# Kernel tuning notes

Measured on AMD Instinct MI355X. Metric: run time of the kernel, lower is better.

Reference implementation:

```python
import jax, jax.numpy as jnp
import numpy as np

NEG = -1e30  # effective -inf in float32, safe under logaddexp grads
EPS = 1e-7   # keras.backend.epsilon()


def _ctc_loss(y_pred, y_true):
    """Faithful port of keras.backend.ctc_batch_cost with full-length
    input_length=T and label_length=L (as the CTCLayer sets them).
    y_pred: [B, T, C] post-softmax probabilities; blank = C-1.
    y_true: [B, L] int labels in [0, C-1).
    Returns loss [B, 1].
    """
    logp = jnp.log(y_pred + EPS)            # keras takes log(prob + eps)
    B, T, C = y_pred.shape
    L = y_true.shape[1]
    S = 2 * L + 1
    blank = C - 1

    # Extended label sequence: blank, l1, blank, l2, ..., blank  -> [B, S]
    ext = jnp.full((B, S), blank, dtype=y_true.dtype).at[:, 1::2].set(y_true)
    # Per-time emission log-probs of extended symbols: [B, T, S]
    lp_ext = jnp.take_along_axis(logp, ext[:, None, :], axis=2)

    # Skip transition s-2 -> s allowed when ext[s] != blank and ext[s] != ext[s-2]
    prev2_ext = jnp.pad(ext[:, :-2], ((0, 0), (2, 0)), constant_values=-1)
    allow_skip = (ext != blank) & (ext != prev2_ext)  # [B, S]

    # alpha init at t=0
    alpha = jnp.full((B, S), NEG, dtype=logp.dtype)
    alpha = alpha.at[:, 0].set(lp_ext[:, 0, 0]).at[:, 1].set(lp_ext[:, 0, 1])

    def step(alpha, lp_t):
        shift1 = jnp.pad(alpha[:, :-1], ((0, 0), (1, 0)), constant_values=NEG)
        shift2 = jnp.pad(alpha[:, :-2], ((0, 0), (2, 0)), constant_values=NEG)
        shift2 = jnp.where(allow_skip, shift2, NEG)
        new = jnp.logaddexp(jnp.logaddexp(alpha, shift1), shift2) + lp_t
        return new, None

    lp_seq = jnp.moveaxis(lp_ext[:, 1:, :], 1, 0)  # [T-1, B, S]
    alpha, _ = jax.lax.scan(step, alpha, lp_seq)

    # Terminate in final blank or final label
    loss = -jnp.logaddexp(alpha[:, S - 1], alpha[:, S - 2])  # [B]
    return loss[:, None]  # keras returns [B, 1]


def setup_inputs() -> dict:
    key = jax.random.key(0)
    k1, k2 = jax.random.split(key)
    B, T, C, L = 256, 256, 1000, 64
    y_true = jax.random.randint(k1, (B, L), 0, C - 1, dtype=jnp.int64)
    logits = jax.random.normal(k2, (B, T, C), dtype=jnp.float32)
    y_pred = jax.nn.softmax(logits, axis=-1)  # module expects softmax probs
    return {"y_true": y_true, "y_pred": y_pred}


def reference(y_true, y_pred):
    return _ctc_loss(y_pred, y_true)
```

## Files before the change

### kernel.cpp

```cpp
#include <hip/hip_runtime.h>


#define T_    256
#define C_    1000
#define L_    64
#define BLANK 999
#define NEGF  (-1e30f)
#define EPSF  (1e-7f)
#define RS    68
#define CK    64
#define NV    17

__global__ __launch_bounds__(256)
void ctc_gather_kernel(const int* __restrict__ y_true,
                       const float* __restrict__ y_pred,
                       float* __restrict__ lp) {
    const int wave = threadIdx.x >> 6;
    const int lane = threadIdx.x & 63;
    const int pair = blockIdx.x * 4 + wave;
    const int b = pair >> 8;

    const int lab = y_true[b * L_ + lane];
    const float* __restrict__ row = y_pred + (size_t)pair * C_;
    float* __restrict__ orow = lp + (size_t)pair * RS;

    float v = row[lab];
    orow[1 + lane] = __logf(v + EPSF);
    if (lane == 0) {
        orow[0] = __logf(row[BLANK] + EPSF);
    }
}

__global__ __launch_bounds__(64)
void ctc_scan_kernel(const int* __restrict__ y_true,
                     const float* __restrict__ lp,
                     float* __restrict__ out) {
    __shared__ float sbuf[2][CK * RS];

    const int b    = blockIdx.x;
    const int lane = threadIdx.x;

    const float* __restrict__ lrow = lp + (size_t)b * T_ * RS;

    const int lab   = y_true[b * L_ + lane];
    const int labm1 = __shfl_up(lab, 1, 64);
    const bool allow = (lane > 0) && (lab != labm1);

    float aE = NEGF, aO = NEGF, aL = NEGF;

    float4 va[NV], vb[NV];

    auto loadChunk = [&](int c, float4 (&v)[NV]) {
        const float4* g = (const float4*)(lrow + (size_t)c * CK * RS);
        #pragma unroll
        for (int k = 0; k < NV; ++k) v[k] = g[k * 64 + lane];
    };
    auto writeChunk = [&](int sel, float4 (&v)[NV]) {
        float4* d = (float4*)&sbuf[sel][0];
        #pragma unroll
        for (int k = 0; k < NV; ++k) d[k * 64 + lane] = v[k];
    };

    auto step = [&](float lpB, float lpL) {
        float upO = __shfl_up(aO, 1, 64);
        if (lane == 0) upO = NEGF;
        float mE = fmaxf(aE, upO);
        float nE = mE + __logf(__expf(aE - mE) + __expf(upO - mE)) + lpB;
        float sk = allow ? upO : NEGF;
        float mO = fmaxf(fmaxf(aO, aE), sk);
        float nO = mO + __logf(__expf(aO - mO) + __expf(aE - mO) +
                               __expf(sk - mO)) + lpL;
        float mL = fmaxf(aL, aO);
        float nL2 = mL + __logf(__expf(aL - mL) + __expf(aO - mL)) + lpB;
        aE = nE; aO = nO; aL = nL2;
    };

    auto scanChunk = [&](int sel, int rlo) {
        const float* B = &sbuf[sel][0];
        float rB0 = B[rlo * RS],       rL0 = B[rlo * RS + 1 + lane];
        float rB1 = B[(rlo + 1) * RS], rL1 = B[(rlo + 1) * RS + 1 + lane];
        for (int j = rlo; j < CK; ++j) {
            float lpB = rB0, lpL = rL0;
            rB0 = rB1; rL0 = rL1;
            int nr = j + 2; if (nr > CK - 1) nr = CK - 1;
            rB1 = B[nr * RS]; rL1 = B[nr * RS + 1 + lane];
            step(lpB, lpL);
        }
    };

    loadChunk(0, va); writeChunk(0, va);
    loadChunk(1, vb);

    aE = (lane == 0) ? sbuf[0][0] : NEGF;
    aO = (lane == 0) ? sbuf[0][1] : NEGF;

    scanChunk(0, 1);
    writeChunk(1, vb);
    loadChunk(2, va);
    scanChunk(1, 0);
    writeChunk(0, va);
    loadChunk(3, vb);
    scanChunk(0, 0);
    writeChunk(1, vb);
    scanChunk(1, 0);

    if (lane == 63) {
        float m = fmaxf(aL, aO);
        out[b] = -(m + __logf(__expf(aL - m) + __expf(aO - m)));
    }
}

extern "C" void kernel_launch(void* const* d_in, const int* in_sizes, int n_in,
                              void* d_out, int out_size, void* d_ws, size_t ws_size,
                              hipStream_t stream) {
    const int*   y_true = (const int*)d_in[0];
    const float* y_pred = (const float*)d_in[1];
    float*       out    = (float*)d_out;
    float*       lp     = (float*)d_ws;
    (void)in_sizes; (void)n_in; (void)ws_size; (void)out_size;

    ctc_gather_kernel<<<dim3((256 * 256) / 4), dim3(256), 0, stream>>>(y_true, y_pred, lp);
    ctc_scan_kernel<<<dim3(256), dim3(64), 0, stream>>>(y_true, lp, out);
}
```

Before: 401.2 us.

## Replace scattered label gather with coalesced row streaming and class-to-slot map

The gather kernel, which read one scattered element per label from each probability row, is replaced by an extract kernel that streams whole rows with coalesced float4 loads. It writes log-probs only for classes present in the label set, using a per-batch byte map from class to a deduplicated slot. The scan kernel then reads each label's log-prob through its first-occurrence slot index, with blank at slot 64. This trades many uncoalesced 4-byte reads for full-row bandwidth (about 1000 floats per row), plus a serial duplicate search in both kernels.

Result: slower. 434.6 us (+8.3%).

```diff
diff --git a/kernel.cpp b/kernel.cpp
--- a/kernel.cpp
+++ b/kernel.cpp
@@ -10,24 +10,55 @@
 #define RS    68
 #define CK    64
 #define NV    17
+#define RPB   32
 
 __global__ __launch_bounds__(256)
-void ctc_gather_kernel(const int* __restrict__ y_true,
-                       const float* __restrict__ y_pred,
-                       float* __restrict__ lp) {
-    const int wave = threadIdx.x >> 6;
-    const int lane = threadIdx.x & 63;
-    const int pair = blockIdx.x * 4 + wave;
-    const int b = pair >> 8;
+void ctc_extract_kernel(const int* __restrict__ y_true,
+                        const float* __restrict__ y_pred,
+                        float* __restrict__ V) {
+    __shared__ int          slab[64];
+    __shared__ unsigned int sm32[256];
 
-    const int lab = y_true[b * L_ + lane];
-    const float* __restrict__ row = y_pred + (size_t)pair * C_;
-    float* __restrict__ orow = lp + (size_t)pair * RS;
+    const int tid = threadIdx.x;
+    const int b   = blockIdx.x >> 3;
+    const int t0  = (blockIdx.x & 7) * RPB;
 
-    float v = row[lab];
-    orow[1 + lane] = __logf(v + EPSF);
-    if (lane == 0) {
-        orow[0] = __logf(row[BLANK] + EPSF);
+    sm32[tid] = 0xFFFFFFFFu;
+    if (tid < 64) slab[tid] = y_true[b * L_ + tid];
+    __syncthreads();
+    if (tid < 64) {
+        const int myl = slab[tid];
+        int fp = tid;
+        for (int j = 0; j < 64; ++j) { if (slab[j] == myl) { fp = j; break; } }
+        if (fp == tid) ((unsigned char*)sm32)[myl] = (unsigned char)tid;
+    }
+    if (tid == 0) ((unsigned char*)sm32)[BLANK] = 64;
+    __syncthreads();
+
+    const bool act = tid < 250;
+    const unsigned int sm = sm32[tid];
+    const float* __restrict__ base = y_pred + ((size_t)b * T_ + t0) * C_;
+
+    for (int r0 = 0; r0 < RPB; r0 += 4) {
+        float4 v[4];
+        #pragma unroll
+        for (int q = 0; q < 4; ++q) {
+            const float* row = base + (size_t)(r0 + q) * C_;
+            v[q] = act ? ((const float4*)row)[tid]
+                       : make_float4(0.f, 0.f, 0.f, 0.f);
+        }
+        if (act && sm != 0xFFFFFFFFu) {
+            #pragma unroll
+            for (int q = 0; q < 4; ++q) {
+                float* orow = V + (size_t)(b * T_ + t0 + r0 + q) * RS;
+                const float vals[4] = { v[q].x, v[q].y, v[q].z, v[q].w };
+                #pragma unroll
+                for (int e = 0; e < 4; ++e) {
+                    const unsigned int sl = (sm >> (8 * e)) & 0xFFu;
+                    if (sl != 0xFFu) orow[sl] = __logf(vals[e] + EPSF);
+                }
+            }
+        }
     }
 }
 
@@ -45,6 +76,12 @@
     const int lab   = y_true[b * L_ + lane];
     const int labm1 = __shfl_up(lab, 1, 64);
     const bool allow = (lane > 0) && (lab != labm1);
+
+    int fp = 64;
+    for (int j = 0; j < 64; ++j) {
+        const int lj = __shfl(lab, j, 64);
+        if (fp == 64 && lj == lab) fp = j;
+    }
 
     float aE = NEGF, aO = NEGF, aL = NEGF;
 
@@ -77,13 +114,13 @@
 
     auto scanChunk = [&](int sel, int rlo) {
         const float* B = &sbuf[sel][0];
-        float rB0 = B[rlo * RS],       rL0 = B[rlo * RS + 1 + lane];
-        float rB1 = B[(rlo + 1) * RS], rL1 = B[(rlo + 1) * RS + 1 + lane];
+        float rB0 = B[rlo * RS + 64],       rL0 = B[rlo * RS + fp];
+        float rB1 = B[(rlo + 1) * RS + 64], rL1 = B[(rlo + 1) * RS + fp];
         for (int j = rlo; j < CK; ++j) {
-            float lpB = rB0, lpL = rL0;
+            const float lpB = rB0, lpL = rL0;
             rB0 = rB1; rL0 = rL1;
             int nr = j + 2; if (nr > CK - 1) nr = CK - 1;
-            rB1 = B[nr * RS]; rL1 = B[nr * RS + 1 + lane];
+            rB1 = B[nr * RS + 64]; rL1 = B[nr * RS + fp];
             step(lpB, lpL);
         }
     };
@@ -91,8 +128,8 @@
     loadChunk(0, va); writeChunk(0, va);
     loadChunk(1, vb);
 
-    aE = (lane == 0) ? sbuf[0][0] : NEGF;
-    aO = (lane == 0) ? sbuf[0][1] : NEGF;
+    aE = (lane == 0) ? sbuf[0][64] : NEGF;
+    aO = (lane == 0) ? sbuf[0][0]  : NEGF;
 
     scanChunk(0, 1);
     writeChunk(1, vb);
@@ -105,7 +142,7 @@
     scanChunk(1, 0);
 
     if (lane == 63) {
-        float m = fmaxf(aL, aO);
+        const float m = fmaxf(aL, aO);
         out[b] = -(m + __logf(__expf(aL - m) + __expf(aO - m)));
     }
 }
@@ -116,9 +153,9 @@
     const int*   y_true = (const int*)d_in[0];
     const float* y_pred = (const float*)d_in[1];
     float*       out    = (float*)d_out;
-    float*       lp     = (float*)d_ws;
+    float*       V      = (float*)d_ws;
     (void)in_sizes; (void)n_in; (void)ws_size; (void)out_size;
 
-    ctc_gather_kernel<<<dim3((256 * 256) / 4), dim3(256), 0, stream>>>(y_true, y_pred, lp);
-    ctc_scan_kernel<<<dim3(256), dim3(64), 0, stream>>>(y_true, lp, out);
+    ctc_extract_kernel<<<dim3(256 * (T_ / RPB)), dim3(256), 0, stream>>>(y_true, y_pred, V);
+    ctc_scan_kernel<<<dim3(256), dim3(64), 0, stream>>>(y_true, V, out);
 }
```
